# Optimization experiments

Hardware: AMD Instinct MI355X
Metric: run time of the kernel (lower is better)

The kernel has to match this reference:

```python
import jax, jax.numpy as jnp
import numpy as np

M = 64      # memory_size
DV = 64     # memory_value_state_dim
DK = 64     # memory_key_state_dim
DQA = 128   # qa_embed_dim
B = 16384


def setup_inputs() -> dict:
    key = jax.random.key(0)
    ks = jax.random.split(key, 16)
    s = 0.05
    return {
        'control_key': jax.random.normal(ks[0], (B, DK), jnp.float32),
        'control_qa': jax.random.normal(ks[1], (B, DQA), jnp.float32),
        'memory_key': jax.random.normal(ks[2], (M, DK), jnp.float32),
        'memory_value': jax.random.normal(ks[3], (B, M, DV), jnp.float32),
        'We': jax.random.normal(ks[4], (DQA, DV), jnp.float32) * s,
        'be': jnp.zeros((DV,), jnp.float32),
        'Wemv': jax.random.normal(ks[5], (M * DV, DV), jnp.float32) * s,
        'bemv': jnp.zeros((DV,), jnp.float32),
        'Wza': jax.random.normal(ks[6], (DV, DV), jnp.float32) * s,
        'bza': jnp.zeros((DV,), jnp.float32),
        'Wamv': jax.random.normal(ks[7], (M * DV, DV), jnp.float32) * s,
        'bamv': jnp.zeros((DV,), jnp.float32),
        'Wc0': jax.random.normal(ks[8], (M * DV, DQA), jnp.float32) * s,
        'bc0': jnp.zeros((DQA,), jnp.float32),
        'Wm1': jax.random.normal(ks[9], (DQA, M * DV), jnp.float32) * s,
        'bm1': jnp.zeros((M * DV,), jnp.float32),
        'Wz': jax.random.normal(ks[10], (DQA, DV), jnp.float32) * s,
        'bz': jnp.zeros((DV,), jnp.float32),
        'Wzmv': jax.random.normal(ks[11], (M * DV, DV), jnp.float32) * s,
        'bzmv': jnp.zeros((DV,), jnp.float32),
    }


def reference(control_key, control_qa, memory_key, memory_value,
              We, be, Wemv, bemv, Wza, bza, Wamv, bamv,
              Wc0, bc0, Wm1, bm1, Wz, bz, Wzmv, bzmv):
    # attention: log_softmax(control_key @ memory_key^T).exp() == softmax
    write_weight = jax.nn.softmax(control_key @ memory_key.T, axis=1)  # [B, M]

    # ---- hyper_write ----
    mem_flat0 = memory_value.reshape(-1, M * DV)                       # [B, M*DV]
    # content_m_round0: Flatten -> Linear -> Sigmoid, gated by control_qa
    content0 = control_qa * jax.nn.sigmoid(mem_flat0 @ Wc0 + bc0)      # [B, DQA]
    # memory_m_round1 gating of memory
    gate1 = jax.nn.sigmoid(content0 @ Wm1 + bm1).reshape(-1, M, DV)
    memory_pre = memory_value * gate1                                  # [B, M, DV]
    mem_flat = memory_pre.reshape(-1, M * DV)

    # erase: sigmoid(erase_net(content0) + erase_mv_net(flat(memory_pre)))
    erase_signal = jax.nn.sigmoid(
        jax.nn.sigmoid(content0 @ We + be)
        + jax.nn.sigmoid(mem_flat @ Wemv + bemv))                      # [B, DV]

    # zt: sigmoid(zt_signal(content0) + zt_signal_Mv(flat(memory_pre)))
    zt = jax.nn.sigmoid((content0 @ Wz + bz) + (mem_flat @ Wzmv + bzmv))

    # add: tanh(zt_add_net(zt) + add_mv_net(flat(memory_pre)))
    add_signal = jnp.tanh(
        jnp.tanh(zt @ Wza + bza) + jnp.tanh(mem_flat @ Wamv + bamv))   # [B, DV]

    # outer-product erase/add update
    w = write_weight[:, :, None]                                       # [B, M, 1]
    erase_mult = 1.0 - w * erase_signal[:, None, :]                     # [B, M, DV]
    aggre_add = w * add_signal[:, None, :]
    new_memory = memory_pre * erase_mult + aggre_add                    # [B, M, DV]
    return new_memory


if __name__ == '__main__':
    out = reference(**setup_inputs())
    print(out.shape)
```

## Files before the change

### kernel.cpp

```cpp
#include <hip/hip_runtime.h>

#define NB  16384
#define MM  64
#define DV  64
#define DK  64
#define DQA 128
#define MD  4096

typedef float  floatx4 __attribute__((ext_vector_type(4)));
typedef short  shortx8 __attribute__((ext_vector_type(8)));

static __device__ __forceinline__ unsigned short f2bf(float f) {
  union { float f; unsigned int u; } v; v.f = f;
  unsigned int r = v.u + 0x7FFFu + ((v.u >> 16) & 1u);
  return (unsigned short)(r >> 16);
}
static __device__ __forceinline__ float bf2f(unsigned short u) {
  union { unsigned int u; float f; } v; v.u = (unsigned int)u << 16; return v.f;
}
static __device__ __forceinline__ float sigm(float x) { return 1.0f / (1.0f + __expf(-x)); }

static __device__ __forceinline__ shortx8 load8bf(const float* p) {
  const float4* p4 = (const float4*)p;
  float4 a = p4[0];
  float4 b = p4[1];
  shortx8 r;
  r[0] = (short)f2bf(a.x); r[1] = (short)f2bf(a.y);
  r[2] = (short)f2bf(a.z); r[3] = (short)f2bf(a.w);
  r[4] = (short)f2bf(b.x); r[5] = (short)f2bf(b.y);
  r[6] = (short)f2bf(b.z); r[7] = (short)f2bf(b.w);
  return r;
}

__global__ __launch_bounds__(256) void k_tr(const float* __restrict__ src,
                                            unsigned short* __restrict__ dst,
                                            int N, int dstld) {
  __shared__ unsigned short T[64 * 72];
  const int k0 = blockIdx.x * 64, n0 = blockIdx.y * 64;
  const int t = threadIdx.x;
#pragma unroll
  for (int i = 0; i < 16; ++i) {
    int idx = t + i * 256, kl = idx >> 6, nl = idx & 63;
    T[kl * 72 + nl] = f2bf(src[(size_t)(k0 + kl) * N + n0 + nl]);
  }
  __syncthreads();
#pragma unroll
  for (int i = 0; i < 16; ++i) {
    int idx = t + i * 256, nl = idx >> 6, kl = idx & 63;
    dst[(size_t)(n0 + nl) * dstld + k0 + kl] = T[kl * 72 + nl];
  }
}

__global__ __launch_bounds__(256) void k_ww(const float* __restrict__ ck,
                                            const float* __restrict__ mk,
                                            float* __restrict__ ww) {
  const int t = threadIdx.x;
  const int lane = t & 63;
  const int wv = t >> 6;
  const int b = blockIdx.x * 4 + wv;
  const float4* ck4 = (const float4*)(ck + (size_t)b * DK);
  const float4* mk4 = (const float4*)(mk + (size_t)lane * DK);
  float s = 0.f;
#pragma unroll
  for (int i = 0; i < DK / 4; ++i) {
    float4 a = ck4[i], m = mk4[i];
    s += a.x * m.x + a.y * m.y + a.z * m.z + a.w * m.w;
  }
  float mx = s;
#pragma unroll
  for (int off = 32; off; off >>= 1) mx = fmaxf(mx, __shfl_xor(mx, off, 64));
  float e = __expf(s - mx);
  float sum = e;
#pragma unroll
  for (int off = 32; off; off >>= 1) sum += __shfl_xor(sum, off, 64);
  ww[(size_t)b * MM + lane] = e / sum;
}

__global__ __launch_bounds__(256) void k_c0(const float* __restrict__ mv,
                                            const unsigned short* __restrict__ WcT,
                                            const float* __restrict__ bc0,
                                            const float* __restrict__ qa,
                                            unsigned short* __restrict__ c0p) {
  __shared__ __align__(16) unsigned short WB[DQA * 136];
  const int t = threadIdx.x, lane = t & 63, wv = t >> 6;
  const int quad = lane >> 4, l16 = lane & 15;
  const int mh = wv & 1, nq2 = wv >> 1;
  const int rowbase = blockIdx.x * 32;
  const int arow = rowbase + mh * 16 + l16;

  floatx4 acc[4];
#pragma unroll
  for (int nt = 0; nt < 4; ++nt) acc[nt] = (floatx4){0.f, 0.f, 0.f, 0.f};

  for (int kc = 0; kc < MD / 128; ++kc) {
    const int kb = kc * 128;
    shortx8 afr[4];
#pragma unroll
    for (int ks = 0; ks < 4; ++ks)
      afr[ks] = load8bf(mv + (size_t)arow * MD + kb + ks * 32 + quad * 8);
#pragma unroll
    for (int i = 0; i < 8; ++i) {
      int idx = t + i * 256;
      int n = idx >> 4, kbk = idx & 15;
      *(shortx8*)&WB[n * 136 + kbk * 8] =
          *(const shortx8*)(WcT + (size_t)n * MD + kb + kbk * 8);
    }
    __syncthreads();
#pragma unroll
    for (int nt = 0; nt < 4; ++nt)
#pragma unroll
      for (int ks = 0; ks < 4; ++ks) {
        shortx8 bfr = *(const shortx8*)&WB[(nq2 * 64 + nt * 16 + l16) * 136 + ks * 32 + quad * 8];
        acc[nt] = __builtin_amdgcn_mfma_f32_16x16x32_bf16(afr[ks], bfr, acc[nt], 0, 0, 0);
      }
    __syncthreads();
  }
#pragma unroll
  for (int nt = 0; nt < 4; ++nt) {
    int col = nq2 * 64 + nt * 16 + l16;
    float b = bc0[col];
#pragma unroll
    for (int r = 0; r < 4; ++r) {
      int row = rowbase + mh * 16 + quad * 4 + r;
      float val = qa[(size_t)row * DQA + col] * sigm(acc[nt][r] + b);
      c0p[(size_t)row * DQA + col] = f2bf(val);
    }
  }
}

__global__ __launch_bounds__(256) void k_g1mp(const float* __restrict__ mv,
                                              const unsigned short* __restrict__ c0p,
                                              const unsigned short* __restrict__ Wm1T,
                                              const float* __restrict__ bm1,
                                              float* __restrict__ mp) {
  __shared__ __align__(16) unsigned short WB[128 * 136];
  const int t = threadIdx.x, lane = t & 63, wv = t >> 6;
  const int quad = lane >> 4, l16 = lane & 15;
  const int rowbase = blockIdx.x * 64;
  const int colbase = blockIdx.y * 128;

  shortx8 c0fr[4];
#pragma unroll
  for (int ks = 0; ks < 4; ++ks)
    c0fr[ks] = *(const shortx8*)(c0p + (size_t)(rowbase + wv * 16 + l16) * DQA + ks * 32 + quad * 8);

#pragma unroll
  for (int i = 0; i < 8; ++i) {
    int idx = t + i * 256;
    int n = idx >> 4, kbk = idx & 15;
    *(shortx8*)&WB[n * 136 + kbk * 8] =
        *(const shortx8*)(Wm1T + (size_t)(colbase + n) * DQA + kbk * 8);
  }
  __syncthreads();

  floatx4 acc[8];
#pragma unroll
  for (int nt = 0; nt < 8; ++nt) acc[nt] = (floatx4){0.f, 0.f, 0.f, 0.f};
#pragma unroll
  for (int nt = 0; nt < 8; ++nt)
#pragma unroll
    for (int ks = 0; ks < 4; ++ks) {
      shortx8 bfr = *(const shortx8*)&WB[(nt * 16 + l16) * 136 + ks * 32 + quad * 8];
      acc[nt] = __builtin_amdgcn_mfma_f32_16x16x32_bf16(c0fr[ks], bfr, acc[nt], 0, 0, 0);
    }

#pragma unroll
  for (int nt = 0; nt < 8; ++nt) {
    int colg = colbase + nt * 16 + l16;
    float b = bm1[colg];
#pragma unroll
    for (int r = 0; r < 4; ++r) {
      int row = rowbase + wv * 16 + quad * 4 + r;
      float g = sigm(acc[nt][r] + b);
      mp[(size_t)row * MD + colg] = mv[(size_t)row * MD + colg] * g;
    }
  }
}

__global__ __launch_bounds__(256) void k_S(const float* __restrict__ mp,
                                           const unsigned short* __restrict__ W3T,
                                           float* __restrict__ Sg) {
  __shared__ __align__(16) unsigned short WB[192 * 136];
  const int t = threadIdx.x, lane = t & 63, wv = t >> 6;
  const int quad = lane >> 4, l16 = lane & 15;
  const int mh = wv & 1, nh2 = wv >> 1;
  const int rowbase = blockIdx.x * 32;
  const int arow = rowbase + mh * 16 + l16;

  floatx4 acc[6];
#pragma unroll
  for (int nt = 0; nt < 6; ++nt) acc[nt] = (floatx4){0.f, 0.f, 0.f, 0.f};

  for (int kc = 0; kc < MD / 128; ++kc) {
    const int kb = kc * 128;
    shortx8 afr[4];
#pragma unroll
    for (int ks = 0; ks < 4; ++ks)
      afr[ks] = load8bf(mp + (size_t)arow * MD + kb + ks * 32 + quad * 8);
#pragma unroll
    for (int i = 0; i < 12; ++i) {
      int idx = t + i * 256;
      int n = idx >> 4, kbk = idx & 15;
      *(shortx8*)&WB[n * 136 + kbk * 8] =
          *(const shortx8*)(W3T + (size_t)n * MD + kb + kbk * 8);
    }
    __syncthreads();
#pragma unroll
    for (int nt = 0; nt < 6; ++nt)
#pragma unroll
      for (int ks = 0; ks < 4; ++ks) {
        shortx8 bfr = *(const shortx8*)&WB[(nh2 * 96 + nt * 16 + l16) * 136 + ks * 32 + quad * 8];
        acc[nt] = __builtin_amdgcn_mfma_f32_16x16x32_bf16(afr[ks], bfr, acc[nt], 0, 0, 0);
      }
    __syncthreads();
  }
#pragma unroll
  for (int nt = 0; nt < 6; ++nt) {
    int col = nh2 * 96 + nt * 16 + l16;
#pragma unroll
    for (int r = 0; r < 4; ++r) {
      int row = rowbase + mh * 16 + quad * 4 + r;
      Sg[(size_t)row * 192 + col] = acc[nt][r];
    }
  }
}

__global__ __launch_bounds__(256) void k_eza(const unsigned short* __restrict__ c0p,
                                             const float* __restrict__ Sg,
                                             const float* __restrict__ We,
                                             const float* __restrict__ be,
                                             const float* __restrict__ Wz,
                                             const float* __restrict__ bz,
                                             const float* __restrict__ Wza,
                                             const float* __restrict__ bza,
                                             const float* __restrict__ bemv,
                                             const float* __restrict__ bzmv,
                                             const float* __restrict__ bamv,
                                             float* __restrict__ eg,
                                             float* __restrict__ ag) {
  __shared__ float ztl[4][64];
  const int t = threadIdx.x;
  const int j = t & 63;
  const int r = t >> 6;
  const int b = blockIdx.x * 4 + r;
  const unsigned short* c0r = c0p + (size_t)b * DQA;
  float ae = 0.f, az = 0.f;
#pragma unroll 8
  for (int k = 0; k < DQA; ++k) {
    float cv = bf2f(c0r[k]);
    ae += cv * We[k * DV + j];
    az += cv * Wz[k * DV + j];
  }
  const float* Sr = Sg + (size_t)b * 192;
  float zt = sigm(az + bz[j] + Sr[64 + j] + bzmv[j]);
  ztl[r][j] = zt;
  __syncthreads();
  float aa = 0.f;
#pragma unroll 8
  for (int k = 0; k < DV; ++k) aa += ztl[r][k] * Wza[k * DV + j];
  float aval = tanhf(tanhf(aa + bza[j]) + tanhf(Sr[128 + j] + bamv[j]));
  float eval = sigm(sigm(ae + be[j]) + sigm(Sr[j] + bemv[j]));
  eg[(size_t)b * DV + j] = eval;
  ag[(size_t)b * DV + j] = aval;
}

__global__ __launch_bounds__(256) void k_final(float* __restrict__ mp,
                                               const float* __restrict__ ww,
                                               const float* __restrict__ eg,
                                               const float* __restrict__ ag) {
  const size_t idx8 = ((size_t)blockIdx.x * 256 + threadIdx.x) * 8;
  const int row = (int)(idx8 >> 12);
  const int colg = (int)(idx8 & 4095);
  const int mi = colg >> 6, j = colg & 63;
  const float w = ww[(size_t)row * MM + mi];
  const float4 e0 = *(const float4*)(eg + (size_t)row * DV + j);
  const float4 e1 = *(const float4*)(eg + (size_t)row * DV + j + 4);
  const float4 a0 = *(const float4*)(ag + (size_t)row * DV + j);
  const float4 a1 = *(const float4*)(ag + (size_t)row * DV + j + 4);
  float4 m0 = *(const float4*)(mp + idx8);
  float4 m1 = *(const float4*)(mp + idx8 + 4);
  m0.x = m0.x * (1.f - w * e0.x) + w * a0.x;
  m0.y = m0.y * (1.f - w * e0.y) + w * a0.y;
  m0.z = m0.z * (1.f - w * e0.z) + w * a0.z;
  m0.w = m0.w * (1.f - w * e0.w) + w * a0.w;
  m1.x = m1.x * (1.f - w * e1.x) + w * a1.x;
  m1.y = m1.y * (1.f - w * e1.y) + w * a1.y;
  m1.z = m1.z * (1.f - w * e1.z) + w * a1.z;
  m1.w = m1.w * (1.f - w * e1.w) + w * a1.w;
  *(float4*)(mp + idx8) = m0;
  *(float4*)(mp + idx8 + 4) = m1;
}

extern "C" void kernel_launch(void* const* d_in, const int* in_sizes, int n_in,
                              void* d_out, int out_size, void* d_ws, size_t ws_size,
                              hipStream_t stream) {
  const float* ck   = (const float*)d_in[0];
  const float* qa   = (const float*)d_in[1];
  const float* mk   = (const float*)d_in[2];
  const float* mv   = (const float*)d_in[3];
  const float* We   = (const float*)d_in[4];
  const float* be   = (const float*)d_in[5];
  const float* Wemv = (const float*)d_in[6];
  const float* bemv = (const float*)d_in[7];
  const float* Wza  = (const float*)d_in[8];
  const float* bza  = (const float*)d_in[9];
  const float* Wamv = (const float*)d_in[10];
  const float* bamv = (const float*)d_in[11];
  const float* Wc0  = (const float*)d_in[12];
  const float* bc0  = (const float*)d_in[13];
  const float* Wm1  = (const float*)d_in[14];
  const float* bm1  = (const float*)d_in[15];
  const float* Wz   = (const float*)d_in[16];
  const float* bz   = (const float*)d_in[17];
  const float* Wzmv = (const float*)d_in[18];
  const float* bzmv = (const float*)d_in[19];
  float* outp = (float*)d_out;

  char* base = (char*)d_ws;
  float* wwp = (float*)base;                      base += (size_t)NB * MM * 4;
  unsigned short* c0p = (unsigned short*)base;    base += (size_t)NB * DQA * 2;
  float* Sp = (float*)base;                       base += (size_t)NB * 192 * 4;
  float* ep = (float*)base;                       base += (size_t)NB * DV * 4;
  float* ap = (float*)base;                       base += (size_t)NB * DV * 4;
  unsigned short* WcT  = (unsigned short*)base;   base += (size_t)DQA * MD * 2;
  unsigned short* Wm1T = (unsigned short*)base;   base += (size_t)MD * DQA * 2;
  unsigned short* W3T  = (unsigned short*)base;   base += (size_t)192 * MD * 2;

  k_tr<<<dim3(MD / 64, DQA / 64), 256, 0, stream>>>(Wc0, WcT, DQA, MD);
  k_tr<<<dim3(DQA / 64, MD / 64), 256, 0, stream>>>(Wm1, Wm1T, MD, DQA);
  k_tr<<<dim3(MD / 64, 1), 256, 0, stream>>>(Wemv, W3T, DV, MD);
  k_tr<<<dim3(MD / 64, 1), 256, 0, stream>>>(Wzmv, W3T + (size_t)64 * MD, DV, MD);
  k_tr<<<dim3(MD / 64, 1), 256, 0, stream>>>(Wamv, W3T + (size_t)128 * MD, DV, MD);

  k_ww<<<NB / 4, 256, 0, stream>>>(ck, mk, wwp);
  k_c0<<<NB / 32, 256, 0, stream>>>(mv, WcT, bc0, qa, c0p);
  k_g1mp<<<dim3(NB / 64, MD / 128), 256, 0, stream>>>(mv, c0p, Wm1T, bm1, outp);
  k_S<<<NB / 32, 256, 0, stream>>>(outp, W3T, Sp);
  k_eza<<<NB / 4, 256, 0, stream>>>(c0p, Sp, We, be, Wz, bz, Wza, bza, bemv, bzmv, bamv, ep, ap);
  k_final<<<(NB * MD / 8) / 256, 256, 0, stream>>>(outp, wwp, ep, ap);
}
```

Before: 1.167 ms.

## Split-K the c0 and S GEMMs in two, pad weight stride, stagger K order

```diff
diff --git a/kernel.cpp b/kernel.cpp
--- a/kernel.cpp
+++ b/kernel.cpp
@@ -6,9 +6,11 @@
 #define DK  64
 #define DQA 128
 #define MD  4096
+#define LDW 4224
 
 typedef float  floatx4 __attribute__((ext_vector_type(4)));
 typedef short  shortx8 __attribute__((ext_vector_type(8)));
+typedef unsigned short ushortx4 __attribute__((ext_vector_type(4)));
 
 static __device__ __forceinline__ unsigned short f2bf(float f) {
   union { float f; unsigned int u; } v; v.f = f;
@@ -78,21 +80,21 @@
 
 __global__ __launch_bounds__(256) void k_c0(const float* __restrict__ mv,
                                             const unsigned short* __restrict__ WcT,
-                                            const float* __restrict__ bc0,
-                                            const float* __restrict__ qa,
-                                            unsigned short* __restrict__ c0p) {
+                                            float* __restrict__ P) {
   __shared__ __align__(16) unsigned short WB[DQA * 136];
   const int t = threadIdx.x, lane = t & 63, wv = t >> 6;
   const int quad = lane >> 4, l16 = lane & 15;
   const int mh = wv & 1, nq2 = wv >> 1;
   const int rowbase = blockIdx.x * 32;
+  const int split = blockIdx.y;
   const int arow = rowbase + mh * 16 + l16;
 
   floatx4 acc[4];
 #pragma unroll
   for (int nt = 0; nt < 4; ++nt) acc[nt] = (floatx4){0.f, 0.f, 0.f, 0.f};
 
-  for (int kc = 0; kc < MD / 128; ++kc) {
+  for (int c = 0; c < 16; ++c) {
+    const int kc = split * 16 + ((c + blockIdx.x) & 15);
     const int kb = kc * 128;
     shortx8 afr[4];
 #pragma unroll
@@ -103,7 +105,7 @@
       int idx = t + i * 256;
       int n = idx >> 4, kbk = idx & 15;
       *(shortx8*)&WB[n * 136 + kbk * 8] =
-          *(const shortx8*)(WcT + (size_t)n * MD + kb + kbk * 8);
+          *(const shortx8*)(WcT + (size_t)n * LDW + kb + kbk * 8);
     }
     __syncthreads();
 #pragma unroll
@@ -115,17 +117,34 @@
       }
     __syncthreads();
   }
+  float* Pp = P + (size_t)split * NB * DQA;
 #pragma unroll
   for (int nt = 0; nt < 4; ++nt) {
     int col = nq2 * 64 + nt * 16 + l16;
-    float b = bc0[col];
 #pragma unroll
     for (int r = 0; r < 4; ++r) {
       int row = rowbase + mh * 16 + quad * 4 + r;
-      float val = qa[(size_t)row * DQA + col] * sigm(acc[nt][r] + b);
-      c0p[(size_t)row * DQA + col] = f2bf(val);
-    }
-  }
+      Pp[(size_t)row * DQA + col] = acc[nt][r];
+    }
+  }
+}
+
+__global__ __launch_bounds__(256) void k_c0fin(const float* __restrict__ P,
+                                               const float* __restrict__ bc0,
+                                               const float* __restrict__ qa,
+                                               unsigned short* __restrict__ c0p) {
+  const size_t i4 = ((size_t)blockIdx.x * 256 + threadIdx.x) * 4;
+  const int col = (int)(i4 & (DQA - 1));
+  float4 p0 = *(const float4*)(P + i4);
+  float4 p1 = *(const float4*)(P + (size_t)NB * DQA + i4);
+  float4 b  = *(const float4*)(bc0 + col);
+  float4 q  = *(const float4*)(qa + i4);
+  ushortx4 o;
+  o[0] = f2bf(q.x * sigm(p0.x + p1.x + b.x));
+  o[1] = f2bf(q.y * sigm(p0.y + p1.y + b.y));
+  o[2] = f2bf(q.z * sigm(p0.z + p1.z + b.z));
+  o[3] = f2bf(q.w * sigm(p0.w + p1.w + b.w));
+  *(ushortx4*)(c0p + i4) = o;
 }
 
 __global__ __launch_bounds__(256) void k_g1mp(const float* __restrict__ mv,
@@ -185,13 +204,15 @@
   const int quad = lane >> 4, l16 = lane & 15;
   const int mh = wv & 1, nh2 = wv >> 1;
   const int rowbase = blockIdx.x * 32;
+  const int split = blockIdx.y;
   const int arow = rowbase + mh * 16 + l16;
 
   floatx4 acc[6];
 #pragma unroll
   for (int nt = 0; nt < 6; ++nt) acc[nt] = (floatx4){0.f, 0.f, 0.f, 0.f};
 
-  for (int kc = 0; kc < MD / 128; ++kc) {
+  for (int c = 0; c < 16; ++c) {
+    const int kc = split * 16 + ((c + blockIdx.x) & 15);
     const int kb = kc * 128;
     shortx8 afr[4];
 #pragma unroll
@@ -202,7 +223,7 @@
       int idx = t + i * 256;
       int n = idx >> 4, kbk = idx & 15;
       *(shortx8*)&WB[n * 136 + kbk * 8] =
-          *(const shortx8*)(W3T + (size_t)n * MD + kb + kbk * 8);
+          *(const shortx8*)(W3T + (size_t)n * LDW + kb + kbk * 8);
     }
     __syncthreads();
 #pragma unroll
@@ -214,13 +235,14 @@
       }
     __syncthreads();
   }
+  float* Sp = Sg + (size_t)split * NB * 192;
 #pragma unroll
   for (int nt = 0; nt < 6; ++nt) {
     int col = nh2 * 96 + nt * 16 + l16;
 #pragma unroll
     for (int r = 0; r < 4; ++r) {
       int row = rowbase + mh * 16 + quad * 4 + r;
-      Sg[(size_t)row * 192 + col] = acc[nt][r];
+      Sp[(size_t)row * 192 + col] = acc[nt][r];
     }
   }
 }
@@ -251,15 +273,16 @@
     ae += cv * We[k * DV + j];
     az += cv * Wz[k * DV + j];
   }
-  const float* Sr = Sg + (size_t)b * 192;
-  float zt = sigm(az + bz[j] + Sr[64 + j] + bzmv[j]);
+  const float* Sr0 = Sg + (size_t)b * 192;
+  const float* Sr1 = Sg + (size_t)NB * 192 + (size_t)b * 192;
+  float zt = sigm(az + bz[j] + Sr0[64 + j] + Sr1[64 + j] + bzmv[j]);
   ztl[r][j] = zt;
   __syncthreads();
   float aa = 0.f;
 #pragma unroll 8
   for (int k = 0; k < DV; ++k) aa += ztl[r][k] * Wza[k * DV + j];
-  float aval = tanhf(tanhf(aa + bza[j]) + tanhf(Sr[128 + j] + bamv[j]));
-  float eval = sigm(sigm(ae + be[j]) + sigm(Sr[j] + bemv[j]));
+  float aval = tanhf(tanhf(aa + bza[j]) + tanhf(Sr0[128 + j] + Sr1[128 + j] + bamv[j]));
+  float eval = sigm(sigm(ae + be[j]) + sigm(Sr0[j] + Sr1[j] + bemv[j]));
   eg[(size_t)b * DV + j] = eval;
   ag[(size_t)b * DV + j] = aval;
 }
@@ -319,23 +342,26 @@
   char* base = (char*)d_ws;
   float* wwp = (float*)base;                      base += (size_t)NB * MM * 4;
   unsigned short* c0p = (unsigned short*)base;    base += (size_t)NB * DQA * 2;
-  float* Sp = (float*)base;                       base += (size_t)NB * 192 * 4;
+  float* Sp = (float*)base;                       base += (size_t)2 * NB * 192 * 4;
   float* ep = (float*)base;                       base += (size_t)NB * DV * 4;
   float* ap = (float*)base;                       base += (size_t)NB * DV * 4;
-  unsigned short* WcT  = (unsigned short*)base;   base += (size_t)DQA * MD * 2;
+  unsigned short* WcT  = (unsigned short*)base;   base += (size_t)DQA * LDW * 2;
   unsigned short* Wm1T = (unsigned short*)base;   base += (size_t)MD * DQA * 2;
-  unsigned short* W3T  = (unsigned short*)base;   base += (size_t)192 * MD * 2;
-
-  k_tr<<<dim3(MD / 64, DQA / 64), 256, 0, stream>>>(Wc0, WcT, DQA, MD);
+  unsigned short* W3T  = (unsigned short*)base;   base += (size_t)192 * LDW * 2;
+
+  float* Pp = outp;
+
+  k_tr<<<dim3(MD / 64, DQA / 64), 256, 0, stream>>>(Wc0, WcT, DQA, LDW);
   k_tr<<<dim3(DQA / 64, MD / 64), 256, 0, stream>>>(Wm1, Wm1T, MD, DQA);
-  k_tr<<<dim3(MD / 64, 1), 256, 0, stream>>>(Wemv, W3T, DV, MD);
-  k_tr<<<dim3(MD / 64, 1), 256, 0, stream>>>(Wzmv, W3T + (size_t)64 * MD, DV, MD);
-  k_tr<<<dim3(MD / 64, 1), 256, 0, stream>>>(Wamv, W3T + (size_t)128 * MD, DV, MD);
+  k_tr<<<dim3(MD / 64, 1), 256, 0, stream>>>(Wemv, W3T, DV, LDW);
+  k_tr<<<dim3(MD / 64, 1), 256, 0, stream>>>(Wzmv, W3T + (size_t)64 * LDW, DV, LDW);
+  k_tr<<<dim3(MD / 64, 1), 256, 0, stream>>>(Wamv, W3T + (size_t)128 * LDW, DV, LDW);
 
   k_ww<<<NB / 4, 256, 0, stream>>>(ck, mk, wwp);
-  k_c0<<<NB / 32, 256, 0, stream>>>(mv, WcT, bc0, qa, c0p);
+  k_c0<<<dim3(NB / 32, 2), 256, 0, stream>>>(mv, WcT, Pp);
+  k_c0fin<<<(NB * DQA / 4) / 256, 256, 0, stream>>>(Pp, bc0, qa, c0p);
   k_g1mp<<<dim3(NB / 64, MD / 128), 256, 0, stream>>>(mv, c0p, Wm1T, bm1, outp);
-  k_S<<<NB / 32, 256, 0, stream>>>(outp, W3T, Sp);
+  k_S<<<dim3(NB / 32, 2), 256, 0, stream>>>(outp, W3T, Sp);
   k_eza<<<NB / 4, 256, 0, stream>>>(c0p, Sp, We, be, Wz, bz, Wza, bza, bemv, bzmv, bamv, ep, ap);
   k_final<<<(NB * MD / 8) / 256, 256, 0, stream>>>(outp, wwp, ep, ap);
 }
```

Measured after the change: 1.047 ms. 10.3% less time.
